# Kernel optimization log

Hardware: AMD Instinct MI355X
Metric: run time of the kernel (lower is better)

The kernel has to match this reference:

```python
import jax, jax.numpy as jnp
import numpy as np

N = 100000
E = 1600000
IN_C = 128
OUT_C = 64
EDGE_DIM = 16
EDGE_HID = 32
EPS = 1e-5


def setup_inputs() -> dict:
    key = jax.random.key(0)
    ks = jax.random.split(key, 12)
    x = jax.random.normal(ks[0], (N, IN_C), dtype=jnp.float32)
    edge_index = jax.random.randint(ks[1], (2, E), 0, N, dtype=jnp.int64)
    edge_attr = jax.random.uniform(ks[2], (E, EDGE_DIM), dtype=jnp.float32)
    # PDNConv params
    lin_w = jax.random.normal(ks[3], (OUT_C, IN_C), dtype=jnp.float32) / np.sqrt(IN_C)
    bias = jnp.zeros((OUT_C,), dtype=jnp.float32)
    mlp_w1 = jax.random.normal(ks[4], (EDGE_HID, EDGE_DIM), dtype=jnp.float32) / np.sqrt(EDGE_DIM)
    mlp_b1 = jnp.zeros((EDGE_HID,), dtype=jnp.float32)
    mlp_w2 = jax.random.normal(ks[5], (1, EDGE_HID), dtype=jnp.float32) / np.sqrt(EDGE_HID)
    mlp_b2 = jnp.zeros((1,), dtype=jnp.float32)
    # PReLU (single shared parameter, torch default init 0.25)
    prelu_a = jnp.asarray(0.25, dtype=jnp.float32)
    # GraphNorm params
    gn_weight = jnp.ones((OUT_C,), dtype=jnp.float32)
    gn_bias = jnp.zeros((OUT_C,), dtype=jnp.float32)
    gn_mean_scale = jnp.ones((OUT_C,), dtype=jnp.float32)
    return {
        "x": x, "edge_index": edge_index, "edge_attr": edge_attr,
        "lin_w": lin_w, "bias": bias,
        "mlp_w1": mlp_w1, "mlp_b1": mlp_b1, "mlp_w2": mlp_w2, "mlp_b2": mlp_b2,
        "prelu_a": prelu_a,
        "gn_weight": gn_weight, "gn_bias": gn_bias, "gn_mean_scale": gn_mean_scale,
    }


def reference(x, edge_index, edge_attr, lin_w, bias, mlp_w1, mlp_b1, mlp_w2, mlp_b2,
              prelu_a, gn_weight, gn_bias, gn_mean_scale):
    n = x.shape[0]
    # --- PDNConv ---
    # edge MLP: Linear -> ReLU -> Linear -> Sigmoid -> scalar gate per edge
    h = jax.nn.relu(edge_attr @ mlp_w1.T + mlp_b1)           # [E, hid]
    ew = jax.nn.sigmoid(h @ mlp_w2.T + mlp_b2)[:, 0]         # [E]
    # add self-loops with weight 1.0
    loop = jnp.arange(n)
    row = jnp.concatenate([edge_index[0], loop])             # source
    col = jnp.concatenate([edge_index[1], loop])             # target
    ew = jnp.concatenate([ew, jnp.ones((n,), dtype=x.dtype)])
    # gcn_norm: D^{-1/2} A D^{-1/2} with weighted degree on targets
    deg = jax.ops.segment_sum(ew, col, num_segments=n)       # [N]
    dinv = jnp.where(deg > 0, jax.lax.rsqrt(deg), 0.0)
    norm = dinv[row] * ew * dinv[col]                        # [E+N]
    xt = x @ lin_w.T                                         # [N, out]
    msgs = norm[:, None] * xt[row]                           # gather + gate
    out = jax.ops.segment_sum(msgs, col, num_segments=n) + bias  # scatter-add
    # --- PReLU ---
    out = jnp.where(out >= 0, out, prelu_a * out)
    # --- GraphNorm (single graph) ---
    mean = out.mean(axis=0)                                  # [out]
    centered = out - gn_mean_scale * mean
    var = jnp.mean(centered * centered, axis=0)
    out = gn_weight * centered * jax.lax.rsqrt(var + EPS) + gn_bias
    return out
```

## Files before the change

### kernel.cpp

```cpp
#include <hip/hip_runtime.h>
#include <hip/hip_fp16.h>
#include <math.h>

#define IN_C   128
#define OUT_C  64
#define EDIM   16
#define EHID   32
#define GN_EPS 1e-5f
#define MAXDEG 48
#define OVFCAP 2048

typedef unsigned long long u64;
typedef unsigned int u32;

__device__ __forceinline__ float dot4(float4 a, float4 b) {
    return a.x * b.x + a.y * b.y + a.z * b.z + a.w * b.w;
}
__device__ __forceinline__ void fma4(float4& a, float s, float4 w) {
    a.x = fmaf(s, w.x, a.x); a.y = fmaf(s, w.y, a.y);
    a.z = fmaf(s, w.z, a.z); a.w = fmaf(s, w.w, a.w);
}
__device__ __forceinline__ float getc(float4 v, int j) {
    return j == 0 ? v.x : j == 1 ? v.y : j == 2 ? v.z : v.w;
}
__device__ __forceinline__ float deg_from(u64 v) {
    return (float)(v & ((1ull << 44) - 1)) * (1.f / 4294967296.f);
}

__global__ void k_init(u64* __restrict__ degcnt, float* __restrict__ sums,
                       u64* __restrict__ ovfcnt, int N) {
    int i = blockIdx.x * 256 + threadIdx.x;
    if (i < N) degcnt[i] = (1ull << 32);
    if (i < 2 * OUT_C) sums[i] = 0.f;
    if (i == 0) *ovfcnt = 0ull;
}

__global__ void k_edge(const float* __restrict__ ea, const int* __restrict__ ei,
                       const float* __restrict__ w1, const float* __restrict__ b1,
                       const float* __restrict__ w2, const float* __restrict__ b2,
                       u64* __restrict__ degcnt, u64* __restrict__ rec,
                       u64* __restrict__ ovfcnt, int4* __restrict__ ovflist, int E) {
    int e = blockIdx.x * 256 + threadIdx.x;
    if (e >= E) return;

    const float4* eav = (const float4*)ea + (size_t)e * 4;
    float4 a0 = eav[0], a1 = eav[1], a2 = eav[2], a3 = eav[3];

    const float4* w1v = (const float4*)w1;
    float z = b2[0];
    #pragma unroll
    for (int j = 0; j < EHID; ++j) {
        float4 q0 = w1v[j * 4 + 0];
        float4 q1 = w1v[j * 4 + 1];
        float4 q2 = w1v[j * 4 + 2];
        float4 q3 = w1v[j * 4 + 3];
        float h = dot4(a0, q0) + dot4(a1, q1) + dot4(a2, q2) + dot4(a3, q3) + b1[j];
        h = fmaxf(h, 0.f);
        z += h * w2[j];
    }
    float ewv = 1.f / (1.f + __expf(-z));

    int row = ei[e];
    int col = ei[E + e];
    u64 inc = (1ull << 44) | (u64)(ewv * 4294967296.0f);
    u64 old = atomicAdd(&degcnt[col], inc);
    int rank = (int)(old >> 44);
    if (rank < MAXDEG) {
        u64 v = (u64)(unsigned)row | ((u64)(unsigned)__float_as_int(ewv) << 32);
        __hip_atomic_store(&rec[(size_t)col * MAXDEG + rank], v,
                           __ATOMIC_RELAXED, __HIP_MEMORY_SCOPE_AGENT);
    } else {
        u64 oi = atomicAdd(ovfcnt, 1ull);
        if (oi < OVFCAP) ovflist[oi] = make_int4(row, col, __float_as_int(ewv), 0);
    }
}

__global__ void k_edge_fb(const float* __restrict__ ea, const int* __restrict__ ei,
                          const float* __restrict__ w1, const float* __restrict__ b1,
                          const float* __restrict__ w2, const float* __restrict__ b2,
                          u64* __restrict__ degcnt, int2* __restrict__ tmp, int E) {
    int e = blockIdx.x * 256 + threadIdx.x;
    if (e >= E) return;
    const float4* eav = (const float4*)ea + (size_t)e * 4;
    float4 a0 = eav[0], a1 = eav[1], a2 = eav[2], a3 = eav[3];
    const float4* w1v = (const float4*)w1;
    float z = b2[0];
    #pragma unroll
    for (int j = 0; j < EHID; ++j) {
        float4 q0 = w1v[j * 4 + 0];
        float4 q1 = w1v[j * 4 + 1];
        float4 q2 = w1v[j * 4 + 2];
        float4 q3 = w1v[j * 4 + 3];
        float h = dot4(a0, q0) + dot4(a1, q1) + dot4(a2, q2) + dot4(a3, q3) + b1[j];
        h = fmaxf(h, 0.f);
        z += h * w2[j];
    }
    float ewv = 1.f / (1.f + __expf(-z));
    int row = ei[e];
    int col = ei[E + e];
    u64 inc = (1ull << 44) | (u64)(ewv * 4294967296.0f);
    u64 old = atomicAdd(&degcnt[col], inc);
    int rank = (int)(old >> 44);
    tmp[e] = make_int2(row | (rank << 17), __float_as_int(ewv));
}

__global__ void k_finish(const u64* __restrict__ degcnt, float* __restrict__ dinv,
                         int* __restrict__ cnt, int N) {
    int i = blockIdx.x * 256 + threadIdx.x;
    if (i < N) {
        u64 v = degcnt[i];
        dinv[i] = rsqrtf(deg_from(v));
        int c = (int)(v >> 44);
        cnt[i] = c < MAXDEG ? c : MAXDEG;
    }
}

__global__ void k_xt(const float* __restrict__ x, const float* __restrict__ lw,
                     const u64* __restrict__ degcnt, __half* __restrict__ xts, int N) {
    __shared__ float swt[IN_C * OUT_C];
    int tid = threadIdx.x;
    for (int i = tid; i < IN_C * OUT_C; i += 256) {
        int k = i >> 6, c = i & 63;
        swt[i] = lw[c * IN_C + k];
    }
    __syncthreads();

    int lane = tid & 63;
    int c4 = lane & 15;
    int rq = lane >> 4;
    int rbase = blockIdx.x * 64 + (tid >> 6) * 16 + rq * 4;

    int r0 = min(rbase + 0, N - 1), r1 = min(rbase + 1, N - 1);
    int r2 = min(rbase + 2, N - 1), r3 = min(rbase + 3, N - 1);
    const float4* x4 = (const float4*)x;
    float4 acc0 = {0,0,0,0}, acc1 = {0,0,0,0}, acc2 = {0,0,0,0}, acc3 = {0,0,0,0};

    #pragma unroll 4
    for (int k4 = 0; k4 < IN_C / 4; ++k4) {
        float4 xv0 = x4[(size_t)r0 * 32 + k4];
        float4 xv1 = x4[(size_t)r1 * 32 + k4];
        float4 xv2 = x4[(size_t)r2 * 32 + k4];
        float4 xv3 = x4[(size_t)r3 * 32 + k4];
        #pragma unroll
        for (int j = 0; j < 4; ++j) {
            float4 wv = *(const float4*)&swt[(k4 * 4 + j) * OUT_C + (c4 << 2)];
            fma4(acc0, getc(xv0, j), wv);
            fma4(acc1, getc(xv1, j), wv);
            fma4(acc2, getc(xv2, j), wv);
            fma4(acc3, getc(xv3, j), wv);
        }
    }
    int cc = c4 << 2;
    #pragma unroll
    for (int i = 0; i < 4; ++i) {
        int r = rbase + i;
        if (r < N) {
            float d = rsqrtf(deg_from(degcnt[r]));
            float4 a = i == 0 ? acc0 : i == 1 ? acc1 : i == 2 ? acc2 : acc3;
            union { __half2 h[2]; uint2 u; } cv;
            cv.h[0] = __floats2half2_rn(a.x * d, a.y * d);
            cv.h[1] = __floats2half2_rn(a.z * d, a.w * d);
            *(uint2*)&xts[(size_t)r * OUT_C + cc] = cv.u;
        }
    }
}

__global__ void k_gather(const u64* __restrict__ rec, const u64* __restrict__ degcnt,
                         const u32* __restrict__ xtsu, const float2* __restrict__ bias2,
                         float2* __restrict__ out2, int N) {
    int tid  = threadIdx.x;
    int lane = tid & 63;
    int node = blockIdx.x * 8 + ((tid >> 6) << 1) + (lane >> 5);
    if (node >= N) return;
    int sl = lane & 31;

    u64 dv = degcnt[node];
    int num = (int)(dv >> 44);
    num = num < MAXDEG ? num : MAXDEG;
    float dinv = rsqrtf(deg_from(dv));
    size_t beg = (size_t)node * MAXDEG;

    u32 selfv = xtsu[((size_t)node << 5) + sl];
    float2 sf = __half22float2(*(__half2*)&selfv);
    float acc0 = sf.x, acc1 = sf.y;

    int j = 0;
    for (; j + 8 <= num; j += 8) {
        u64 rc[8];
        #pragma unroll
        for (int u = 0; u < 8; ++u) rc[u] = rec[beg + j + u];
        u32 v[8];
        #pragma unroll
        for (int u = 0; u < 8; ++u)
            v[u] = xtsu[((size_t)(u32)rc[u] << 5) + sl];
        #pragma unroll
        for (int u = 0; u < 8; ++u) {
            float w = __int_as_float((int)(rc[u] >> 32));
            float2 f = __half22float2(*(__half2*)&v[u]);
            acc0 = fmaf(w, f.x, acc0);
            acc1 = fmaf(w, f.y, acc1);
        }
    }
    for (; j < num; ++j) {
        u64 rc = rec[beg + j];
        u32 v = xtsu[((size_t)(u32)rc << 5) + sl];
        float w = __int_as_float((int)(rc >> 32));
        float2 f = __half22float2(*(__half2*)&v);
        acc0 = fmaf(w, f.x, acc0);
        acc1 = fmaf(w, f.y, acc1);
    }
    float2 b = bias2[sl];
    out2[((size_t)node << 5) + sl] = make_float2(b.x + dinv * acc0, b.y + dinv * acc1);
}

__global__ void k_ovf(const int4* __restrict__ ovflist, const u64* __restrict__ ovfcnt,
                      const u64* __restrict__ degcnt, const __half* __restrict__ xts,
                      float* __restrict__ out) {
    u64 nv = *ovfcnt;
    int n = nv > (u64)OVFCAP ? OVFCAP : (int)nv;
    int lane = threadIdx.x & 63;
    for (int i = blockIdx.x * 4 + (threadIdx.x >> 6); i < n; i += gridDim.x * 4) {
        int4 v = ovflist[i];
        float w = rsqrtf(deg_from(degcnt[v.y])) * __int_as_float(v.z);
        atomicAdd(&out[(size_t)v.y * OUT_C + lane],
                  w * __half2float(xts[(size_t)v.x * OUT_C + lane]));
    }
}

__global__ void k_init_out(const float* __restrict__ bias, const float* __restrict__ dinv,
                           const __half* __restrict__ xts, float* __restrict__ out, int total) {
    int t = blockIdx.x * 256 + threadIdx.x;
    if (t >= total) return;
    int i = t >> 6, c = t & 63;
    out[t] = bias[c] + dinv[i] * __half2float(xts[t]);
}
__global__ void k_scatter(const int* __restrict__ ei, const int2* __restrict__ tmp,
                          const float* __restrict__ dinv, const __half* __restrict__ xts,
                          float* __restrict__ out, int E) {
    int t = blockIdx.x * 256 + threadIdx.x;
    int e = t >> 6;
    if (e >= E) return;
    int lane = t & 63;
    int2 tm = tmp[e];
    int row = tm.x & 0x1FFFF;
    int col = ei[E + e];
    float w = dinv[col] * __int_as_float(tm.y);
    atomicAdd(out + (size_t)col * OUT_C + lane,
              w * __half2float(xts[(size_t)row * OUT_C + lane]));
}

__global__ void k_stats(const float* __restrict__ out, const float* __restrict__ pa,
                        float* __restrict__ sums, int total) {
    __shared__ float r1[256], r2[256];
    float a = pa[0];
    float s = 0.f, s2 = 0.f;
    int stride = gridDim.x * 256;
    for (int t = blockIdx.x * 256 + threadIdx.x; t < total; t += stride) {
        float v = out[t];
        float y = v >= 0.f ? v : a * v;
        s += y; s2 += y * y;
    }
    int tid = threadIdx.x;
    r1[tid] = s; r2[tid] = s2;
    __syncthreads();
    if (tid < 64) {
        float t1 = r1[tid] + r1[tid + 64] + r1[tid + 128] + r1[tid + 192];
        float t2 = r2[tid] + r2[tid + 64] + r2[tid + 128] + r2[tid + 192];
        atomicAdd(&sums[tid], t1);
        atomicAdd(&sums[OUT_C + tid], t2);
    }
}
__global__ void k_apply(float* __restrict__ out, const float* __restrict__ pa,
                        const float* __restrict__ sums,
                        const float* __restrict__ gw, const float* __restrict__ gb,
                        const float* __restrict__ gms, int total, float invN) {
    int t = blockIdx.x * 256 + threadIdx.x;
    if (t >= total) return;
    int c = t & 63;
    float a  = pa[0];
    float m  = sums[c] * invN;
    float ms = gms[c];
    float var = sums[OUT_C + c] * invN - ms * m * m * (2.f - ms);
    float A = gw[c] * rsqrtf(var + GN_EPS);
    float v = out[t];
    float y = v >= 0.f ? v : a * v;
    out[t] = A * (y - ms * m) + gb[c];
}

extern "C" void kernel_launch(void* const* d_in, const int* in_sizes, int n_in,
                              void* d_out, int out_size, void* d_ws, size_t ws_size,
                              hipStream_t stream) {
    (void)n_in; (void)out_size;
    const float* x    = (const float*)d_in[0];
    const int*   ei   = (const int*)  d_in[1];
    const float* ea   = (const float*)d_in[2];
    const float* lw   = (const float*)d_in[3];
    const float* bias = (const float*)d_in[4];
    const float* w1   = (const float*)d_in[5];
    const float* b1   = (const float*)d_in[6];
    const float* w2   = (const float*)d_in[7];
    const float* b2   = (const float*)d_in[8];
    const float* pa   = (const float*)d_in[9];
    const float* gw   = (const float*)d_in[10];
    const float* gb   = (const float*)d_in[11];
    const float* gms  = (const float*)d_in[12];
    float* out = (float*)d_out;

    int N = in_sizes[0] / IN_C;
    int E = in_sizes[2] / EDIM;
    int total = N * OUT_C;
    int nbN = (N + 255) / 256;
    int nbE = (E + 255) / 256;

    char* p = (char*)d_ws;
    u64*   degcnt = (u64*)p;  p += sizeof(u64) * (size_t)N;
    float* dinv   = (float*)p; p += sizeof(float) * (size_t)N;
    __half* xts   = (__half*)p; p += sizeof(__half) * (size_t)N * OUT_C;
    float* sums   = (float*)p; p += sizeof(float) * 128;
    int*   cnt    = (int*)p;   p += sizeof(int) * (size_t)N;
    char*  tail = p;
    u64*   ovfcnt  = (u64*)tail;
    int4*  ovflist = (int4*)(tail + sizeof(u64) * 2);
    u64*   rec     = (u64*)(tail + sizeof(u64) * 2 + sizeof(int4) * OVFCAP);
    size_t need_csr = (size_t)((char*)(rec + (size_t)N * MAXDEG) - (char*)d_ws);
    int2*  tmp = (int2*)tail;
    bool use_csr = (need_csr <= ws_size);

    if (use_csr) {
        k_init  <<<nbN, 256, 0, stream>>>(degcnt, sums, ovfcnt, N);
        k_edge  <<<nbE, 256, 0, stream>>>(ea, ei, w1, b1, w2, b2, degcnt,
                                          rec, ovfcnt, ovflist, E);
        k_xt    <<<(N + 63) / 64, 256, 0, stream>>>(x, lw, degcnt, xts, N);
        k_gather<<<(N + 7) / 8, 256, 0, stream>>>(rec, degcnt, (const u32*)xts,
                                                  (const float2*)bias, (float2*)out, N);
        k_ovf   <<<64, 256, 0, stream>>>(ovflist, ovfcnt, degcnt, xts, out);
        k_stats <<<512, 256, 0, stream>>>(out, pa, sums, total);
        k_apply <<<(total + 255) / 256, 256, 0, stream>>>(out, pa, sums, gw, gb, gms,
                                                          total, 1.0f / (float)N);
    } else {
        k_init   <<<nbN, 256, 0, stream>>>(degcnt, sums, (u64*)sums , N);
        k_edge_fb<<<nbE, 256, 0, stream>>>(ea, ei, w1, b1, w2, b2, degcnt, tmp, E);
        k_finish <<<nbN, 256, 0, stream>>>(degcnt, dinv, cnt, N);
        k_xt_fb: ;
        k_xt     <<<(N + 63) / 64, 256, 0, stream>>>(x, lw, degcnt, xts, N);
        k_init_out<<<(total + 255) / 256, 256, 0, stream>>>(bias, dinv, xts, out, total);
        long st = (long)E * 64;
        k_scatter <<<(unsigned)((st + 255) / 256), 256, 0, stream>>>(ei, tmp, dinv, xts, out, E);
        k_stats  <<<512, 256, 0, stream>>>(out, pa, sums, total);
        k_apply  <<<(total + 255) / 256, 256, 0, stream>>>(out, pa, sums, gw, gb, gms,
                                                           total, 1.0f / (float)N);
    }
}
```

Baseline: 423.6 us.

## Pack edge records into 32 bits and widen gather lanes to four channels

Each per-target edge record now packs a 17-bit source index and a 15-bit quantized gate into one 32-bit word instead of a 64-bit pair. This halves the record array's storage and the traffic for writing and reading it. The gather kernel now uses 16 lanes per node, each loading 8 bytes of fp16 features and writing a float4, so each block handles twice as many nodes. The cost is quantization error on the edge weights and a hard limit of 2^17 on the number of nodes.

```diff
diff --git a/kernel.cpp b/kernel.cpp
--- a/kernel.cpp
+++ b/kernel.cpp
@@ -38,7 +38,7 @@
 __global__ void k_edge(const float* __restrict__ ea, const int* __restrict__ ei,
                        const float* __restrict__ w1, const float* __restrict__ b1,
                        const float* __restrict__ w2, const float* __restrict__ b2,
-                       u64* __restrict__ degcnt, u64* __restrict__ rec,
+                       u64* __restrict__ degcnt, u32* __restrict__ rec,
                        u64* __restrict__ ovfcnt, int4* __restrict__ ovflist, int E) {
     int e = blockIdx.x * 256 + threadIdx.x;
     if (e >= E) return;
@@ -66,7 +66,9 @@
     u64 old = atomicAdd(&degcnt[col], inc);
     int rank = (int)(old >> 44);
     if (rank < MAXDEG) {
-        u64 v = (u64)(unsigned)row | ((u64)(unsigned)__float_as_int(ewv) << 32);
+        u32 q = (u32)__float2uint_rn(ewv * 32768.f);
+        q = q > 32767u ? 32767u : q;
+        u32 v = (u32)row | (q << 17);
         __hip_atomic_store(&rec[(size_t)col * MAXDEG + rank], v,
                            __ATOMIC_RELAXED, __HIP_MEMORY_SCOPE_AGENT);
     } else {
@@ -165,14 +167,14 @@
     }
 }
 
-__global__ void k_gather(const u64* __restrict__ rec, const u64* __restrict__ degcnt,
-                         const u32* __restrict__ xtsu, const float2* __restrict__ bias2,
-                         float2* __restrict__ out2, int N) {
+__global__ void k_gather(const u32* __restrict__ rec, const u64* __restrict__ degcnt,
+                         const uint2* __restrict__ xtsu2, const float4* __restrict__ bias4,
+                         float4* __restrict__ out4, int N) {
     int tid  = threadIdx.x;
     int lane = tid & 63;
-    int node = blockIdx.x * 8 + ((tid >> 6) << 1) + (lane >> 5);
+    int node = blockIdx.x * 16 + ((tid >> 6) << 2) + (lane >> 4);
     if (node >= N) return;
-    int sl = lane & 31;
+    int sl = lane & 15;
 
     u64 dv = degcnt[node];
     int num = (int)(dv >> 44);
@@ -180,37 +182,46 @@
     float dinv = rsqrtf(deg_from(dv));
     size_t beg = (size_t)node * MAXDEG;
 
-    u32 selfv = xtsu[((size_t)node << 5) + sl];
-    float2 sf = __half22float2(*(__half2*)&selfv);
-    float acc0 = sf.x, acc1 = sf.y;
+    uint2 selfv = xtsu2[((size_t)node << 4) + sl];
+    float2 s0 = __half22float2(*(__half2*)&selfv.x);
+    float2 s1 = __half22float2(*(__half2*)&selfv.y);
+    float acc0 = s0.x, acc1 = s0.y, acc2 = s1.x, acc3 = s1.y;
 
     int j = 0;
     for (; j + 8 <= num; j += 8) {
-        u64 rc[8];
+        u32 rc[8];
         #pragma unroll
         for (int u = 0; u < 8; ++u) rc[u] = rec[beg + j + u];
-        u32 v[8];
+        uint2 v[8];
         #pragma unroll
         for (int u = 0; u < 8; ++u)
-            v[u] = xtsu[((size_t)(u32)rc[u] << 5) + sl];
+            v[u] = xtsu2[((size_t)(rc[u] & 0x1FFFF) << 4) + sl];
         #pragma unroll
         for (int u = 0; u < 8; ++u) {
-            float w = __int_as_float((int)(rc[u] >> 32));
-            float2 f = __half22float2(*(__half2*)&v[u]);
-            acc0 = fmaf(w, f.x, acc0);
-            acc1 = fmaf(w, f.y, acc1);
+            float w = (float)(rc[u] >> 17) * (1.f / 32768.f);
+            float2 f0 = __half22float2(*(__half2*)&v[u].x);
+            float2 f1 = __half22float2(*(__half2*)&v[u].y);
+            acc0 = fmaf(w, f0.x, acc0);
+            acc1 = fmaf(w, f0.y, acc1);
+            acc2 = fmaf(w, f1.x, acc2);
+            acc3 = fmaf(w, f1.y, acc3);
         }
     }
     for (; j < num; ++j) {
-        u64 rc = rec[beg + j];
-        u32 v = xtsu[((size_t)(u32)rc << 5) + sl];
-        float w = __int_as_float((int)(rc >> 32));
-        float2 f = __half22float2(*(__half2*)&v);
-        acc0 = fmaf(w, f.x, acc0);
-        acc1 = fmaf(w, f.y, acc1);
-    }
-    float2 b = bias2[sl];
-    out2[((size_t)node << 5) + sl] = make_float2(b.x + dinv * acc0, b.y + dinv * acc1);
+        u32 rc = rec[beg + j];
+        uint2 v = xtsu2[((size_t)(rc & 0x1FFFF) << 4) + sl];
+        float w = (float)(rc >> 17) * (1.f / 32768.f);
+        float2 f0 = __half22float2(*(__half2*)&v.x);
+        float2 f1 = __half22float2(*(__half2*)&v.y);
+        acc0 = fmaf(w, f0.x, acc0);
+        acc1 = fmaf(w, f0.y, acc1);
+        acc2 = fmaf(w, f1.x, acc2);
+        acc3 = fmaf(w, f1.y, acc3);
+    }
+    float4 b = bias4[sl];
+    out4[((size_t)node << 4) + sl] =
+        make_float4(b.x + dinv * acc0, b.y + dinv * acc1,
+                    b.z + dinv * acc2, b.w + dinv * acc3);
 }
 
 __global__ void k_ovf(const int4* __restrict__ ovflist, const u64* __restrict__ ovfcnt,
@@ -321,7 +332,7 @@
     char*  tail = p;
     u64*   ovfcnt  = (u64*)tail;
     int4*  ovflist = (int4*)(tail + sizeof(u64) * 2);
-    u64*   rec     = (u64*)(tail + sizeof(u64) * 2 + sizeof(int4) * OVFCAP);
+    u32*   rec     = (u32*)(tail + sizeof(u64) * 2 + sizeof(int4) * OVFCAP);
     size_t need_csr = (size_t)((char*)(rec + (size_t)N * MAXDEG) - (char*)d_ws);
     int2*  tmp = (int2*)tail;
     bool use_csr = (need_csr <= ws_size);
@@ -331,8 +342,8 @@
         k_edge  <<<nbE, 256, 0, stream>>>(ea, ei, w1, b1, w2, b2, degcnt,
                                           rec, ovfcnt, ovflist, E);
         k_xt    <<<(N + 63) / 64, 256, 0, stream>>>(x, lw, degcnt, xts, N);
-        k_gather<<<(N + 7) / 8, 256, 0, stream>>>(rec, degcnt, (const u32*)xts,
-                                                  (const float2*)bias, (float2*)out, N);
+        k_gather<<<(N + 15) / 16, 256, 0, stream>>>(rec, degcnt, (const uint2*)xts,
+                                                    (const float4*)bias, (float4*)out, N);
         k_ovf   <<<64, 256, 0, stream>>>(ovflist, ovfcnt, degcnt, xts, out);
         k_stats <<<512, 256, 0, stream>>>(out, pa, sums, total);
         k_apply <<<(total + 255) / 256, 256, 0, stream>>>(out, pa, sums, gw, gb, gms,
@@ -341,7 +352,6 @@
         k_init   <<<nbN, 256, 0, stream>>>(degcnt, sums, (u64*)sums , N);
         k_edge_fb<<<nbE, 256, 0, stream>>>(ea, ei, w1, b1, w2, b2, degcnt, tmp, E);
         k_finish <<<nbN, 256, 0, stream>>>(degcnt, dinv, cnt, N);
-        k_xt_fb: ;
         k_xt     <<<(N + 63) / 64, 256, 0, stream>>>(x, lw, degcnt, xts, N);
         k_init_out<<<(total + 255) / 256, 256, 0, stream>>>(bias, dinv, xts, out, total);
         long st = (long)E * 64;
```

Result: faster. 414.4 us (-2.2%).
